# Performance work log

Measured on AMD Instinct MI355X. Metric: run time of the kernel, lower is better.

The kernel has to match this reference:

```python
import jax, jax.numpy as jnp
import numpy as np

K = 3
STRIDE = 1
PAD = 1


def _bilinear_gather(x, ys, xs):
    # x: [B,C,H,W]; ys, xs: [B,n,Ho,Wo] float sample positions. Zero padding outside.
    B, C, H, W = x.shape
    y0 = jnp.floor(ys)
    x0 = jnp.floor(xs)
    wy1 = ys - y0
    wx1 = xs - x0
    x_flat = x.reshape(B, C, H * W)

    def corner(yc, xc, w):
        valid = (yc >= 0) & (yc <= H - 1) & (xc >= 0) & (xc <= W - 1)
        yi = jnp.clip(yc, 0, H - 1).astype(jnp.int32)
        xi = jnp.clip(xc, 0, W - 1).astype(jnp.int32)
        idx = (yi * W + xi).reshape(B, 1, -1)
        vals = jnp.take_along_axis(x_flat, jnp.broadcast_to(idx, (B, C, idx.shape[-1])), axis=2)
        vals = vals.reshape(B, C, *ys.shape[1:])  # [B,C,n,Ho,Wo]
        return vals * (w * valid)[:, None]

    return (corner(y0, x0, (1 - wy1) * (1 - wx1))
            + corner(y0, x0 + 1, (1 - wy1) * wx1)
            + corner(y0 + 1, x0, wy1 * (1 - wx1))
            + corner(y0 + 1, x0 + 1, wy1 * wx1))


def setup_inputs() -> dict:
    key = jax.random.key(0)
    k1, k2, k3, k4 = jax.random.split(key, 4)
    B, Cin, Cout, H, W = 16, 128, 128, 64, 64
    n = K * K
    x = jax.random.normal(k1, (B, Cin, H, W), dtype=jnp.float32)
    # main deform-conv weight (kaiming-ish scale) and bias
    fan_in = Cin * n
    weight = jax.random.normal(k2, (Cout, Cin, K, K), dtype=jnp.float32) * np.float32(np.sqrt(2.0 / fan_in))
    bias = jnp.zeros((Cout,), dtype=jnp.float32)
    # offset/mask predicting conv (small init so offsets are modest)
    off_w = jax.random.normal(k3, (3 * n, Cin, K, K), dtype=jnp.float32) * np.float32(0.01)
    off_b = jax.random.normal(k4, (3 * n,), dtype=jnp.float32) * np.float32(0.01)
    return {"x": x, "weight": weight, "bias": bias, "off_w": off_w, "off_b": off_b}


def reference(x, weight, bias, off_w, off_b):
    B, Cin, H, W = x.shape
    Cout = weight.shape[0]
    n = K * K
    Ho = (H + 2 * PAD - K) // STRIDE + 1
    Wo = (W + 2 * PAD - K) // STRIDE + 1

    # offset / mask prediction conv
    out = jax.lax.conv_general_dilated(
        x, off_w, window_strides=(STRIDE, STRIDE), padding=((PAD, PAD), (PAD, PAD)),
        dimension_numbers=("NCHW", "OIHW", "NCHW"))
    out = out + off_b[None, :, None, None]  # [B, 3n, Ho, Wo]
    offset = out[:, :2 * n].reshape(B, n, 2, Ho, Wo)  # per-tap (dy, dx)
    mask = jax.nn.sigmoid(out[:, 2 * n:])  # [B, n, Ho, Wo]

    # base sampling grid per kernel tap
    t = jnp.arange(n)
    py = (t // K).astype(jnp.float32)[:, None] + (jnp.arange(Ho) * STRIDE - PAD).astype(jnp.float32)[None, :]  # [n,Ho]
    px = (t % K).astype(jnp.float32)[:, None] + (jnp.arange(Wo) * STRIDE - PAD).astype(jnp.float32)[None, :]   # [n,Wo]
    ys = py[None, :, :, None] + offset[:, :, 0]  # [B,n,Ho,Wo]
    xs = px[None, :, None, :] + offset[:, :, 1]

    sampled = _bilinear_gather(x, ys, xs)            # [B,C,n,Ho,Wo]
    sampled = sampled * mask[:, None]                # modulated (DCNv2)
    w = weight.reshape(Cout, Cin, n)
    y = jnp.einsum("bcnhw,ocn->bohw", sampled, w)
    return y + bias[None, :, None, None]
```

## Files before the change

### kernel.cpp

```cpp
#include <hip/hip_runtime.h>
#include <hip/hip_fp16.h>


typedef unsigned int u32;
typedef __attribute__((ext_vector_type(8))) _Float16 f16x8;
typedef __attribute__((ext_vector_type(4))) float f32x4;

union U16 { uint4 u; f16x8 h; };
union H2U { __half2 h2; u32 u; };

static __device__ __forceinline__ u32 pkh(float a, float b) {
    H2U c; c.h2 = __float22half2_rn(make_float2(a, b)); return c.u;
}
static __device__ __forceinline__ u32 pkw(float w) {
    __half h = __float2half_rn(w);
    H2U c; c.h2 = __half2(h, h); return c.u;
}
static __device__ __forceinline__ u32 hfma2u(u32 a, u32 w, u32 acc) {
    H2U x, y, z; x.u = a; y.u = w; z.u = acc;
    z.h2 = __hfma2(x.h2, y.h2, z.h2); return z.u;
}
static __device__ __forceinline__ u32 hmul2u(u32 a, u32 w) {
    H2U x, y; x.u = a; y.u = w;
    y.h2 = __hmul2(x.h2, y.h2); return y.u;
}

#define B_   16
#define HW_  4096
#define CU_  64

__global__ __launch_bounds__(256) void k_transprep(const float* __restrict__ x,
                                                   u32* __restrict__ xtu,
                                                   const float* __restrict__ weight,
                                                   const float* __restrict__ off_w,
                                                   uint4* __restrict__ wtv,
                                                   u32* __restrict__ woffu) {
    int blk = blockIdx.x, t = threadIdx.x;
    if (blk < 2048) {
        __shared__ float tile[32][130];
        int b = blk >> 7, hw0 = (blk & 127) << 5;
        int hwl = t & 31, cg = t >> 5;
        const float* src = x + (size_t)b * 128 * HW_ + hw0 + hwl;
#pragma unroll
        for (int i = 0; i < 16; ++i) { int c = cg + (i << 3); tile[hwl][c] = src[(size_t)c * HW_]; }
        __syncthreads();
        u32* dst = xtu + ((size_t)b * HW_ + hw0) * CU_;
        int u = t & 63, hq = t >> 6;
#pragma unroll
        for (int j = 0; j < 8; ++j) {
            int hw = (hq << 3) + j;
            float2 rd = *(const float2*)&tile[hw][2 * u];
            dst[(size_t)hw * CU_ + u] = pkh(rd.x, rd.y);
        }
    } else {
        int idx = (blk - 2048) * 256 + t;
        if (idx < 18432) {
            int l = idx & 63, og = (idx >> 6) & 7, ks = (idx >> 9) & 3, n = idx >> 11;
            int o = og * 16 + (l & 15);
            int c0 = ks * 32 + (l >> 4) * 8;
            u32 r[4];
#pragma unroll
            for (int q = 0; q < 4; ++q) {
                int c = c0 + 2 * q;
                r[q] = pkh(weight[((size_t)(o * 128 + c)) * 9 + n],
                           weight[((size_t)(o * 128 + c + 1)) * 9 + n]);
            }
            wtv[idx] = make_uint4(r[0], r[1], r[2], r[3]);
        } else if (idx < 36864) {
            int k = idx - 18432;
            int o = k / 576, r = k % 576;
            int tap = r / 64, cu = r % 64, c = cu * 2;
            u32 v = 0u;
            if (o < 27) {
                float a = off_w[((size_t)(o * 128 + c)) * 9 + tap];
                float b = off_w[((size_t)(o * 128 + c + 1)) * 9 + tap];
                v = pkh(a, b);
            }
            woffu[k] = v;
        }
    }
}

__global__ __launch_bounds__(512) void k_offconv(const u32* __restrict__ xtu,
                                                 const u32* __restrict__ woffu,
                                                 const float* __restrict__ off_b,
                                                 u32* __restrict__ params) {
    __shared__ __align__(16) u32 S4[4][64][64];
    __shared__ float OFF[2][27][65];
    int raw = blockIdx.x;
    int blk = ((raw & 7) << 6) + (raw >> 3);
    int t = threadIdx.x;
    int b = blk >> 5, rp = blk & 31, ho0 = rp << 1;
    const u32* xb = xtu + (size_t)b * HW_ * CU_;
#pragma unroll
    for (int i = 0; i < 8; ++i) {
        int idx = t + (i << 9);
        int r = idx >> 10, rem = idx & 1023;
        int px = rem >> 4, ch = rem & 15;
        int phys = min(max(ho0 - 1 + r, 0), 63);
        uint4 v = *(const uint4*)(xb + ((phys << 6) + px) * CU_ + (ch << 2));
        *(uint4*)&S4[r][px][(ch ^ (px & 7)) << 2] = v;
    }
    __syncthreads();
    int lane = t & 63, w = t >> 6, l15 = lane & 15, lhi = lane >> 4;
    int g = w >> 2, ob = (w >> 1) & 1, pb0 = (w & 1) << 1;
    const uint4 z4 = {0u, 0u, 0u, 0u};
    f32x4 acc[2];
    acc[0] = (f32x4){0.f, 0.f, 0.f, 0.f};
    acc[1] = (f32x4){0.f, 0.f, 0.f, 0.f};
#pragma unroll 1
    for (int tap = 0; tap < 9; ++tap) {
        int ky = tap / 3, kx = tap % 3;
        int yy = ho0 + g + ky - 1;
        if ((unsigned)yy >= 64u) continue;
        int br = g + ky;
        U16 af[4];
#pragma unroll
        for (int ks = 0; ks < 4; ++ks)
            af[ks].u = *(const uint4*)(woffu + (size_t)(ob * 16 + l15) * 576
                                       + tap * 64 + ks * 16 + lhi * 4);
#pragma unroll
        for (int pp = 0; pp < 2; ++pp) {
            int pr = ((pb0 + pp) << 4) + l15;
            int pxs = pr + kx - 1;
            bool v = (unsigned)pxs < 64u;
            int pxc = v ? pxs : 0;
#pragma unroll
            for (int ks = 0; ks < 4; ++ks) {
                U16 sf;
                sf.u = v ? *(const uint4*)&S4[br][pxc][((ks * 4 + lhi) ^ (pxc & 7)) << 2] : z4;
                acc[pp] = __builtin_amdgcn_mfma_f32_16x16x32_f16(af[ks].h, sf.h, acc[pp], 0, 0, 0);
            }
        }
    }
#pragma unroll
    for (int pp = 0; pp < 2; ++pp)
#pragma unroll
        for (int r = 0; r < 4; ++r) {
            int o = ob * 16 + lhi * 4 + r;
            if (o < 27) {
                float s = acc[pp][r] + off_b[o];
                if (o >= 18) s = 1.f / (1.f + __expf(-s));
                OFF[g][o][((pb0 + pp) << 4) + l15] = s;
            }
        }
    __syncthreads();
#pragma unroll 1
    for (int it = 0; it < 3; ++it) {
        int item = it * 512 + t;
        if (item < 1152) {
            int g2 = item >= 576;
            int rem = item - 576 * g2;
            int tap = rem >> 6, px = rem & 63;
            int ho = ho0 + g2;
            float dy = OFF[g2][2 * tap][px];
            float dx = OFF[g2][2 * tap + 1][px];
            float m  = OFF[g2][18 + tap][px];
            float ys = (float)(ho + tap / 3 - 1) + dy;
            float xs = (float)(px + tap % 3 - 1) + dx;
            float y0f = floorf(ys), x0f = floorf(xs);
            float fy = ys - y0f, fx = xs - x0f;
            int y0 = (int)y0f, x0 = (int)x0f;
            bool vy0 = (unsigned)y0 < 64u, vy1 = (unsigned)(y0 + 1) < 64u;
            bool vx0 = (unsigned)x0 < 64u, vx1 = (unsigned)(x0 + 1) < 64u;
            u32 w00p = pkw((vy0 && vx0) ? (1.f - fy) * (1.f - fx) * m : 0.f);
            u32 w01p = pkw((vy0 && vx1) ? (1.f - fy) * fx * m : 0.f);
            u32 w10p = pkw((vy1 && vx0) ? fy * (1.f - fx) * m : 0.f);
            u32 w11p = pkw((vy1 && vx1) ? fy * fx * m : 0.f);
            int y0c = min(max(y0, 0), 63), y1c = min(max(y0 + 1, 0), 63);
            int x0c = min(max(x0, 0), 63), x1c = min(max(x0 + 1, 0), 63);
            u32 a0 = ((u32)y0c << 6) | (u32)x0c;
            u32 a1 = ((u32)y1c << 6) | (u32)x1c;
            u32* dst = params + ((size_t)((b << 6) + ho) * 9 + tap) * 512 + ((px >> 3) << 6);
            *(uint4*)&dst[(px & 7) << 2] = make_uint4(w00p, w01p, w10p, w11p);
            dst[32 + (px & 7)] = a0 | (a1 << 12);
        }
    }
}

__global__ __launch_bounds__(512, 4) void k_fused(const u32* __restrict__ xtu,
                                                  const uint4* __restrict__ wtv,
                                                  const u32* __restrict__ params,
                                                  const float* __restrict__ bias,
                                                  float* __restrict__ out) {
    __shared__ __align__(16) u32 S[2][64][68];
    __shared__ __align__(16) u32 PRM[8][2][64];
    int blk = ((blockIdx.x & 7) << 7) + (blockIdx.x >> 3);
    int t = threadIdx.x;
    int b = blk >> 6, ho = blk & 63;
    int w = t >> 6, lane = t & 63, l15 = lane & 15, lhi = lane >> 4;
    int o0 = w << 4;
    int lane4 = lane << 2;

    f32x4 acc[4];
#pragma unroll
    for (int pb = 0; pb < 4; ++pb) acc[pb] = (f32x4){0.f, 0.f, 0.f, 0.f};

    const char* xbb = (const char*)(xtu + (size_t)b * HW_ * CU_);
    const u32* pP = params + (size_t)(((b << 6) + ho) * 9) * 512 + (w << 6) + lane;

    u32 ld[8][4];

#define ISSUE_G(NB)                                                          \
    _Pragma("unroll") for (int j = 0; j < 8; ++j) {                          \
        u32 A = PRM[w][NB][32 + j];                                          \
        u32 a0 = (A & 0xFFFu) << 8;                                          \
        u32 a1 = ((A >> 12) & 0xFFFu) << 8;                                  \
        u32 a01 = (a0 & ~0x3FFFu) | (a1 & 0x3FFFu);                          \
        u32 a10 = (a1 & ~0x3FFFu) | (a0 & 0x3FFFu);                          \
        ld[j][0] = *(const u32*)(xbb + a0 + lane4);                          \
        ld[j][1] = *(const u32*)(xbb + a01 + lane4);                         \
        ld[j][2] = *(const u32*)(xbb + a10 + lane4);                         \
        ld[j][3] = *(const u32*)(xbb + a1 + lane4);                          \
    }

    PRM[w][0][lane] = pP[0];
    __builtin_amdgcn_sched_barrier(0);
    ISSUE_G(0);
    u32 prNext = pP[512];

#pragma unroll 1
    for (int n = 0; n < 9; ++n) {
        int buf = n & 1;
        U16 wf[4];
#pragma unroll
        for (int ks = 0; ks < 4; ++ks)
            wf[ks].u = wtv[(((n << 2) + ks) * 8 + w) * 64 + lane];
        __builtin_amdgcn_sched_barrier(0);
#pragma unroll
        for (int j = 0; j < 8; ++j) {
            uint4 ww = *(const uint4*)&PRM[w][buf][j << 2];
            u32 r = hfma2u(ld[j][3], ww.w, hfma2u(ld[j][2], ww.z,
                    hfma2u(ld[j][1], ww.y, hmul2u(ld[j][0], ww.x))));
            S[buf][(w << 3) + j][lane] = r;
        }
        if (n < 8) PRM[w][buf ^ 1][lane] = prNext;
        if (n < 7) prNext = pP[(size_t)(n + 2) * 512];
        if (n < 8) { ISSUE_G(buf ^ 1); }
        asm volatile("s_waitcnt lgkmcnt(0)" ::: "memory");
        __builtin_amdgcn_sched_barrier(0);
        __builtin_amdgcn_s_barrier();
        __builtin_amdgcn_sched_barrier(0);
        __builtin_amdgcn_s_setprio(1);
#pragma unroll
        for (int ks = 0; ks < 4; ++ks) {
            U16 sf[4];
#pragma unroll
            for (int pb = 0; pb < 4; ++pb)
                sf[pb].u = *(const uint4*)&S[buf][pb * 16 + l15][(ks * 4 + lhi) << 2];
#pragma unroll
            for (int pb = 0; pb < 4; ++pb)
                acc[pb] = __builtin_amdgcn_mfma_f32_16x16x32_f16(
                    wf[ks].h, sf[pb].h, acc[pb], 0, 0, 0);
        }
        __builtin_amdgcn_s_setprio(0);
    }
#undef ISSUE_G
    float* ob_base = out + (size_t)b * 128 * HW_ + ho * 64;
#pragma unroll
    for (int r = 0; r < 4; ++r) {
        int o = o0 + lhi * 4 + r;
        float bv = bias[o];
#pragma unroll
        for (int pb = 0; pb < 4; ++pb)
            ob_base[(size_t)o * HW_ + pb * 16 + l15] = acc[pb][r] + bv;
    }
}

extern "C" void kernel_launch(void* const* d_in, const int* in_sizes, int n_in,
                              void* d_out, int out_size, void* d_ws, size_t ws_size,
                              hipStream_t stream) {
    const float* x      = (const float*)d_in[0];
    const float* weight = (const float*)d_in[1];
    const float* bias   = (const float*)d_in[2];
    const float* off_w  = (const float*)d_in[3];
    const float* off_b  = (const float*)d_in[4];
    float* out = (float*)d_out;

    u32*   xtu    = (u32*)d_ws;
    uint4* wtv    = (uint4*)(xtu + (size_t)B_ * HW_ * CU_);
    u32*   woffu  = (u32*)wtv + 294912;
    u32*   params = woffu + 18432;

    hipLaunchKernelGGL(k_transprep, dim3(2048 + 144), dim3(256), 0, stream,
                       x, xtu, weight, off_w, wtv, woffu);
    hipLaunchKernelGGL(k_offconv, dim3(512), dim3(512), 0, stream, xtu, woffu, off_b, params);
    hipLaunchKernelGGL(k_fused, dim3(1024), dim3(512), 0, stream, xtu, wtv, params, bias, out);
}
```

Before: 87.54 us.

## Fuse offset-prediction conv into main deformable conv kernel, keep params in LDS

```diff
diff --git a/kernel.cpp b/kernel.cpp
--- a/kernel.cpp
+++ b/kernel.cpp
@@ -81,110 +81,14 @@
     }
 }
 
-__global__ __launch_bounds__(512) void k_offconv(const u32* __restrict__ xtu,
-                                                 const u32* __restrict__ woffu,
-                                                 const float* __restrict__ off_b,
-                                                 u32* __restrict__ params) {
-    __shared__ __align__(16) u32 S4[4][64][64];
-    __shared__ float OFF[2][27][65];
-    int raw = blockIdx.x;
-    int blk = ((raw & 7) << 6) + (raw >> 3);
-    int t = threadIdx.x;
-    int b = blk >> 5, rp = blk & 31, ho0 = rp << 1;
-    const u32* xb = xtu + (size_t)b * HW_ * CU_;
-#pragma unroll
-    for (int i = 0; i < 8; ++i) {
-        int idx = t + (i << 9);
-        int r = idx >> 10, rem = idx & 1023;
-        int px = rem >> 4, ch = rem & 15;
-        int phys = min(max(ho0 - 1 + r, 0), 63);
-        uint4 v = *(const uint4*)(xb + ((phys << 6) + px) * CU_ + (ch << 2));
-        *(uint4*)&S4[r][px][(ch ^ (px & 7)) << 2] = v;
-    }
-    __syncthreads();
-    int lane = t & 63, w = t >> 6, l15 = lane & 15, lhi = lane >> 4;
-    int g = w >> 2, ob = (w >> 1) & 1, pb0 = (w & 1) << 1;
-    const uint4 z4 = {0u, 0u, 0u, 0u};
-    f32x4 acc[2];
-    acc[0] = (f32x4){0.f, 0.f, 0.f, 0.f};
-    acc[1] = (f32x4){0.f, 0.f, 0.f, 0.f};
-#pragma unroll 1
-    for (int tap = 0; tap < 9; ++tap) {
-        int ky = tap / 3, kx = tap % 3;
-        int yy = ho0 + g + ky - 1;
-        if ((unsigned)yy >= 64u) continue;
-        int br = g + ky;
-        U16 af[4];
-#pragma unroll
-        for (int ks = 0; ks < 4; ++ks)
-            af[ks].u = *(const uint4*)(woffu + (size_t)(ob * 16 + l15) * 576
-                                       + tap * 64 + ks * 16 + lhi * 4);
-#pragma unroll
-        for (int pp = 0; pp < 2; ++pp) {
-            int pr = ((pb0 + pp) << 4) + l15;
-            int pxs = pr + kx - 1;
-            bool v = (unsigned)pxs < 64u;
-            int pxc = v ? pxs : 0;
-#pragma unroll
-            for (int ks = 0; ks < 4; ++ks) {
-                U16 sf;
-                sf.u = v ? *(const uint4*)&S4[br][pxc][((ks * 4 + lhi) ^ (pxc & 7)) << 2] : z4;
-                acc[pp] = __builtin_amdgcn_mfma_f32_16x16x32_f16(af[ks].h, sf.h, acc[pp], 0, 0, 0);
-            }
-        }
-    }
-#pragma unroll
-    for (int pp = 0; pp < 2; ++pp)
-#pragma unroll
-        for (int r = 0; r < 4; ++r) {
-            int o = ob * 16 + lhi * 4 + r;
-            if (o < 27) {
-                float s = acc[pp][r] + off_b[o];
-                if (o >= 18) s = 1.f / (1.f + __expf(-s));
-                OFF[g][o][((pb0 + pp) << 4) + l15] = s;
-            }
-        }
-    __syncthreads();
-#pragma unroll 1
-    for (int it = 0; it < 3; ++it) {
-        int item = it * 512 + t;
-        if (item < 1152) {
-            int g2 = item >= 576;
-            int rem = item - 576 * g2;
-            int tap = rem >> 6, px = rem & 63;
-            int ho = ho0 + g2;
-            float dy = OFF[g2][2 * tap][px];
-            float dx = OFF[g2][2 * tap + 1][px];
-            float m  = OFF[g2][18 + tap][px];
-            float ys = (float)(ho + tap / 3 - 1) + dy;
-            float xs = (float)(px + tap % 3 - 1) + dx;
-            float y0f = floorf(ys), x0f = floorf(xs);
-            float fy = ys - y0f, fx = xs - x0f;
-            int y0 = (int)y0f, x0 = (int)x0f;
-            bool vy0 = (unsigned)y0 < 64u, vy1 = (unsigned)(y0 + 1) < 64u;
-            bool vx0 = (unsigned)x0 < 64u, vx1 = (unsigned)(x0 + 1) < 64u;
-            u32 w00p = pkw((vy0 && vx0) ? (1.f - fy) * (1.f - fx) * m : 0.f);
-            u32 w01p = pkw((vy0 && vx1) ? (1.f - fy) * fx * m : 0.f);
-            u32 w10p = pkw((vy1 && vx0) ? fy * (1.f - fx) * m : 0.f);
-            u32 w11p = pkw((vy1 && vx1) ? fy * fx * m : 0.f);
-            int y0c = min(max(y0, 0), 63), y1c = min(max(y0 + 1, 0), 63);
-            int x0c = min(max(x0, 0), 63), x1c = min(max(x0 + 1, 0), 63);
-            u32 a0 = ((u32)y0c << 6) | (u32)x0c;
-            u32 a1 = ((u32)y1c << 6) | (u32)x1c;
-            u32* dst = params + ((size_t)((b << 6) + ho) * 9 + tap) * 512 + ((px >> 3) << 6);
-            *(uint4*)&dst[(px & 7) << 2] = make_uint4(w00p, w01p, w10p, w11p);
-            dst[32 + (px & 7)] = a0 | (a1 << 12);
-        }
-    }
-}
-
-__global__ __launch_bounds__(512, 4) void k_fused(const u32* __restrict__ xtu,
+__global__ __launch_bounds__(512, 6) void k_fused(const u32* __restrict__ xtu,
                                                   const uint4* __restrict__ wtv,
-                                                  const u32* __restrict__ params,
+                                                  const u32* __restrict__ woffu,
+                                                  const float* __restrict__ off_b,
                                                   const float* __restrict__ bias,
                                                   float* __restrict__ out) {
     __shared__ __align__(16) u32 S[2][64][68];
-    __shared__ __align__(16) u32 PRM[8][2][64];
+    __shared__ __align__(16) u32 paramsL[9 * 512];
     int blk = ((blockIdx.x & 7) << 7) + (blockIdx.x >> 3);
     int t = threadIdx.x;
     int b = blk >> 6, ho = blk & 63;
@@ -192,18 +96,92 @@
     int o0 = w << 4;
     int lane4 = lane << 2;
 
+    const u32* xb = xtu + (size_t)b * HW_ * CU_;
+    const char* xbb = (const char*)xb;
+
+    {
+        int ob1 = w & 1, pb1 = w >> 1;
+        f32x4 acc1 = (f32x4){0.f, 0.f, 0.f, 0.f};
+#pragma unroll 1
+        for (int n = 0; n < 9; ++n) {
+            int oy = n / 3 - 1, ox = n % 3 - 1;
+            int yy = ho + oy;
+            bool rowv = (unsigned)yy < 64u;
+            int yyc = min(max(yy, 0), 63);
+#pragma unroll
+            for (int j = 0; j < 8; ++j) {
+                int px = (w << 3) + j;
+                int xx = px + ox;
+                bool v = rowv && ((unsigned)xx < 64u);
+                int xxc = min(max(xx, 0), 63);
+                u32 val = xb[(yyc << 12) + (xxc << 6) + lane];
+                S[0][(w << 3) + j][lane] = v ? val : 0u;
+            }
+            __syncthreads();
+            U16 af2[4];
+#pragma unroll
+            for (int ks = 0; ks < 4; ++ks)
+                af2[ks].u = *(const uint4*)(woffu + (size_t)(ob1 * 16 + l15) * 576
+                                            + n * 64 + ks * 16 + lhi * 4);
+#pragma unroll
+            for (int ks = 0; ks < 4; ++ks) {
+                U16 sfp;
+                sfp.u = *(const uint4*)&S[0][pb1 * 16 + l15][(ks * 4 + lhi) << 2];
+                acc1 = __builtin_amdgcn_mfma_f32_16x16x32_f16(af2[ks].h, sfp.h, acc1, 0, 0, 0);
+            }
+            __syncthreads();
+        }
+        float (*OFF)[65] = (float (*)[65])(&S[1][0][0]);
+#pragma unroll
+        for (int r = 0; r < 4; ++r) {
+            int oo = ob1 * 16 + lhi * 4 + r;
+            if (oo < 27) {
+                float s = acc1[r] + off_b[oo];
+                if (oo >= 18) s = 1.f / (1.f + __expf(-s));
+                OFF[oo][pb1 * 16 + l15] = s;
+            }
+        }
+        __syncthreads();
+#pragma unroll
+        for (int it = 0; it < 2; ++it) {
+            int item = it * 512 + t;
+            if (item < 576) {
+                int tap = item >> 6, px = item & 63;
+                float dy = OFF[2 * tap][px];
+                float dx = OFF[2 * tap + 1][px];
+                float m  = OFF[18 + tap][px];
+                float ys = (float)(ho + tap / 3 - 1) + dy;
+                float xs = (float)(px + tap % 3 - 1) + dx;
+                float y0f = floorf(ys), x0f = floorf(xs);
+                float fy = ys - y0f, fx = xs - x0f;
+                int y0 = (int)y0f, x0 = (int)x0f;
+                bool vy0 = (unsigned)y0 < 64u, vy1 = (unsigned)(y0 + 1) < 64u;
+                bool vx0 = (unsigned)x0 < 64u, vx1 = (unsigned)(x0 + 1) < 64u;
+                u32 w00p = pkw((vy0 && vx0) ? (1.f - fy) * (1.f - fx) * m : 0.f);
+                u32 w01p = pkw((vy0 && vx1) ? (1.f - fy) * fx * m : 0.f);
+                u32 w10p = pkw((vy1 && vx0) ? fy * (1.f - fx) * m : 0.f);
+                u32 w11p = pkw((vy1 && vx1) ? fy * fx * m : 0.f);
+                int y0c = min(max(y0, 0), 63), y1c = min(max(y0 + 1, 0), 63);
+                int x0c = min(max(x0, 0), 63), x1c = min(max(x0 + 1, 0), 63);
+                u32 a0 = ((u32)y0c << 6) | (u32)x0c;
+                u32 a1 = ((u32)y1c << 6) | (u32)x1c;
+                u32* dst = paramsL + tap * 512 + ((px >> 3) << 6);
+                *(uint4*)&dst[(px & 7) << 2] = make_uint4(w00p, w01p, w10p, w11p);
+                dst[32 + (px & 7)] = a0 | (a1 << 12);
+            }
+        }
+        __syncthreads();
+    }
+
     f32x4 acc[4];
 #pragma unroll
     for (int pb = 0; pb < 4; ++pb) acc[pb] = (f32x4){0.f, 0.f, 0.f, 0.f};
-
-    const char* xbb = (const char*)(xtu + (size_t)b * HW_ * CU_);
-    const u32* pP = params + (size_t)(((b << 6) + ho) * 9) * 512 + (w << 6) + lane;
 
     u32 ld[8][4];
 
 #define ISSUE_G(NB)                                                          \
     _Pragma("unroll") for (int j = 0; j < 8; ++j) {                          \
-        u32 A = PRM[w][NB][32 + j];                                          \
+        u32 A = paramsL[(NB) * 512 + (w << 6) + 32 + j];                     \
         u32 a0 = (A & 0xFFFu) << 8;                                          \
         u32 a1 = ((A >> 12) & 0xFFFu) << 8;                                  \
         u32 a01 = (a0 & ~0x3FFFu) | (a1 & 0x3FFFu);                          \
@@ -214,10 +192,7 @@
         ld[j][3] = *(const u32*)(xbb + a1 + lane4);                          \
     }
 
-    PRM[w][0][lane] = pP[0];
-    __builtin_amdgcn_sched_barrier(0);
     ISSUE_G(0);
-    u32 prNext = pP[512];
 
 #pragma unroll 1
     for (int n = 0; n < 9; ++n) {
@@ -229,14 +204,12 @@
         __builtin_amdgcn_sched_barrier(0);
 #pragma unroll
         for (int j = 0; j < 8; ++j) {
-            uint4 ww = *(const uint4*)&PRM[w][buf][j << 2];
+            uint4 ww = *(const uint4*)&paramsL[n * 512 + (w << 6) + (j << 2)];
             u32 r = hfma2u(ld[j][3], ww.w, hfma2u(ld[j][2], ww.z,
                     hfma2u(ld[j][1], ww.y, hmul2u(ld[j][0], ww.x))));
             S[buf][(w << 3) + j][lane] = r;
         }
-        if (n < 8) PRM[w][buf ^ 1][lane] = prNext;
-        if (n < 7) prNext = pP[(size_t)(n + 2) * 512];
-        if (n < 8) { ISSUE_G(buf ^ 1); }
+        if (n < 8) { ISSUE_G(n + 1); }
         asm volatile("s_waitcnt lgkmcnt(0)" ::: "memory");
         __builtin_amdgcn_sched_barrier(0);
         __builtin_amdgcn_s_barrier();
@@ -280,10 +253,9 @@
     u32*   xtu    = (u32*)d_ws;
     uint4* wtv    = (uint4*)(xtu + (size_t)B_ * HW_ * CU_);
     u32*   woffu  = (u32*)wtv + 294912;
-    u32*   params = woffu + 18432;
 
     hipLaunchKernelGGL(k_transprep, dim3(2048 + 144), dim3(256), 0, stream,
                        x, xtu, weight, off_w, wtv, woffu);
-    hipLaunchKernelGGL(k_offconv, dim3(512), dim3(512), 0, stream, xtu, woffu, off_b, params);
-    hipLaunchKernelGGL(k_fused, dim3(1024), dim3(512), 0, stream, xtu, wtv, params, bias, out);
-}
+    hipLaunchKernelGGL(k_fused, dim3(1024), dim3(512), 0, stream,
+                       xtu, wtv, woffu, off_b, bias, out);
+}
```

After: 158.2 us. +80.7%, slower.
